# Optimization experiments

Measured on AMD Instinct MI355X. Metric: run time of the kernel, lower is better.

## Reference

```python
import jax, jax.numpy as jnp
import numpy as np

N = 100000
C = 128
H = 8
D = C // H  # head_dim = 16
E = 640000


def setup_inputs() -> dict:
    key = jax.random.key(0)
    ks = jax.random.split(key, 10)
    s = 1.0 / np.sqrt(C)
    return {
        "features": jax.random.normal(ks[0], (N, C), dtype=jnp.float32),
        "edge_index": jax.random.randint(ks[1], (2, E), 0, N, dtype=jnp.int64),
        "Wq": jax.random.uniform(ks[2], (C, C), jnp.float32, -s, s),
        "bq": jnp.zeros((C,), jnp.float32),
        "Wk": jax.random.uniform(ks[3], (C, C), jnp.float32, -s, s),
        "bk": jnp.zeros((C,), jnp.float32),
        "Wv": jax.random.uniform(ks[4], (C, C), jnp.float32, -s, s),
        "bv": jnp.zeros((C,), jnp.float32),
        "Wo": jax.random.uniform(ks[5], (C, C), jnp.float32, -s, s),
        "bo": jnp.zeros((C,), jnp.float32),
    }


def reference(features, edge_index, Wq, bq, Wk, bk, Wv, bv, Wo, bo):
    row, col = edge_index[0], edge_index[1]  # [E], [E]
    # Linear projections (torch Linear: x @ W.T + b), reshape to heads
    q = (features @ Wq.T + bq).reshape(N, H, D)
    k = (features @ Wk.T + bk).reshape(N, H, D)
    v = (features @ Wv.T + bv).reshape(N, H, D)
    # Per-edge dot-product scores [E, H]
    attn = jnp.einsum('ehd,ehd->eh', q[row], k[col]) / jnp.sqrt(jnp.float32(D))
    # Faithful to original: softmax over ALL edges (dim=0), per head
    attn = jax.nn.softmax(attn, axis=0)
    # Weighted scatter-add of source values into destination nodes
    msgs = attn[:, :, None] * v[col]  # [E, H, D]
    out = jax.ops.segment_sum(msgs, row, num_segments=N)  # [N, H, D]
    out = out.reshape(N, C)
    return out @ Wo.T + bo
```

## Files before the change

kernel.cpp:

```cpp
#include <hip/hip_runtime.h>


#define TPB 256

typedef __attribute__((ext_vector_type(8))) short short8;
typedef __attribute__((ext_vector_type(4))) short short4v;
typedef __attribute__((ext_vector_type(4))) float f32x4;

__device__ __forceinline__ short f2bf(float f) {
    unsigned u = __float_as_uint(f);
    u += 0x7fffu + ((u >> 16) & 1u);
    return (short)(u >> 16);
}
__device__ __forceinline__ float bf2f(short s) {
    return __uint_as_float(((unsigned)(unsigned short)s) << 16);
}

__global__ void wconv_kernel(const float* __restrict__ W0, const float* __restrict__ W1,
                             const float* __restrict__ W2, const float* __restrict__ W3,
                             short* __restrict__ out)
{
    int i = blockIdx.x * TPB + threadIdx.x;
    if (i >= 65536) return;
    const float* W = (i < 16384) ? W0 : (i < 32768) ? W1 : (i < 49152) ? W2 : W3;
    out[i] = f2bf(W[i & 16383]);
}

template<bool IN_BF16, bool OUT_BF16>
__device__ __forceinline__ void gemm_body(
    const void* __restrict__ Xv, int nrows,
    const short* __restrict__ Wb, const float* __restrict__ bias,
    void* __restrict__ Yv, int xblk)
{
    __shared__ short lw[16384];
    const int tid = threadIdx.x;

    short8 wreg[8];
    #pragma unroll
    for (int r = 0; r < 8; ++r) {
        int c = r * 256 + tid;
        int fragid = c >> 6, ln = c & 63;
        int n = fragid >> 2, kc = fragid & 3;
        wreg[r] = *(const short8*)&Wb[(n*16 + (ln & 15))*128 + kc*32 + (ln >> 4)*8];
    }

    const int wid = tid >> 6;
    const int lane = tid & 63;
    const int l15 = lane & 15;
    const int lh  = lane >> 4;
    const int rowbase = xblk * 128 + wid * 32;
    const int r0 = rowbase + l15, r1 = r0 + 16;
    const bool vv0 = r0 < nrows, vv1 = r1 < nrows;

    short8 xfr[4][2];
    if (IN_BF16) {
        const short* Xb = (const short*)Xv;
        #pragma unroll
        for (int kc = 0; kc < 4; ++kc) {
            xfr[kc][0] = vv0 ? *(const short8*)&Xb[(size_t)r0*128 + kc*32 + lh*8]
                             : (short8)(short)0;
            xfr[kc][1] = vv1 ? *(const short8*)&Xb[(size_t)r1*128 + kc*32 + lh*8]
                             : (short8)(short)0;
        }
    } else {
        const float* Xf = (const float*)Xv;
        const float4* P0 = (const float4*)(Xf + (size_t)r0 * 128);
        const float4* P1 = (const float4*)(Xf + (size_t)r1 * 128);
        float4 xa[4][2], xb[4][2];
        #pragma unroll
        for (int kc = 0; kc < 4; ++kc) {
            xa[kc][0] = vv0 ? P0[kc*8 + lh*2]     : make_float4(0.f,0.f,0.f,0.f);
            xb[kc][0] = vv0 ? P0[kc*8 + lh*2 + 1] : make_float4(0.f,0.f,0.f,0.f);
            xa[kc][1] = vv1 ? P1[kc*8 + lh*2]     : make_float4(0.f,0.f,0.f,0.f);
            xb[kc][1] = vv1 ? P1[kc*8 + lh*2 + 1] : make_float4(0.f,0.f,0.f,0.f);
        }
        #pragma unroll
        for (int kc = 0; kc < 4; ++kc)
            #pragma unroll
            for (int g = 0; g < 2; ++g) {
                xfr[kc][g][0] = f2bf(xa[kc][g].x);
                xfr[kc][g][1] = f2bf(xa[kc][g].y);
                xfr[kc][g][2] = f2bf(xa[kc][g].z);
                xfr[kc][g][3] = f2bf(xa[kc][g].w);
                xfr[kc][g][4] = f2bf(xb[kc][g].x);
                xfr[kc][g][5] = f2bf(xb[kc][g].y);
                xfr[kc][g][6] = f2bf(xb[kc][g].z);
                xfr[kc][g][7] = f2bf(xb[kc][g].w);
            }
    }

    #pragma unroll
    for (int r = 0; r < 8; ++r)
        *(short8*)&lw[(r * 256 + tid) * 8] = wreg[r];
    __syncthreads();

    f32x4 acc[8][2];
    #pragma unroll
    for (int n = 0; n < 8; ++n) { acc[n][0] = (f32x4)0.f; acc[n][1] = (f32x4)0.f; }

    #pragma unroll
    for (int kc = 0; kc < 4; ++kc) {
        short8 wf[8];
        #pragma unroll
        for (int n = 0; n < 8; ++n)
            wf[n] = *(const short8*)&lw[((n*4 + kc)*64 + lane) * 8];
        #pragma unroll
        for (int n = 0; n < 8; ++n) {
            acc[n][0] = __builtin_amdgcn_mfma_f32_16x16x32_bf16(wf[n], xfr[kc][0], acc[n][0], 0, 0, 0);
            acc[n][1] = __builtin_amdgcn_mfma_f32_16x16x32_bf16(wf[n], xfr[kc][1], acc[n][1], 0, 0, 0);
        }
    }

    #pragma unroll
    for (int g = 0; g < 2; ++g) {
        int row = rowbase + g*16 + l15;
        if (row >= nrows) continue;
        #pragma unroll
        for (int n = 0; n < 8; ++n) {
            float4 b4 = *(const float4*)&bias[n*16 + lh*4];
            float y0 = acc[n][g][0] + b4.x;
            float y1 = acc[n][g][1] + b4.y;
            float y2 = acc[n][g][2] + b4.z;
            float y3 = acc[n][g][3] + b4.w;
            if (OUT_BF16) {
                short4v s; s[0]=f2bf(y0); s[1]=f2bf(y1); s[2]=f2bf(y2); s[3]=f2bf(y3);
                *(short4v*)&((short*)Yv)[(size_t)row * 128 + n*16 + lh*4] = s;
            } else {
                *(float4*)&((float*)Yv)[(size_t)row * 128 + n*16 + lh*4] =
                    make_float4(y0, y1, y2, y3);
            }
        }
    }
}

__global__ __launch_bounds__(256) void gemm_out_kernel(
    const short* __restrict__ Xb, int nrows,
    const short* __restrict__ Wb, const float* __restrict__ bias,
    float* __restrict__ Y)
{
    gemm_body<true, false>(Xb, nrows, Wb, bias, Y, blockIdx.x);
}

__global__ __launch_bounds__(256) void gemm_qkv_kernel(
    const float* __restrict__ X, int nrows, int nxblk,
    const short* __restrict__ WB,
    const float* __restrict__ bq, const float* __restrict__ bk,
    const float* __restrict__ bv,
    short* __restrict__ Yb, size_t slice)
{
    int b = blockIdx.x;
    int k = b & 7, j = b >> 3;
    int jd = j / 3, w = j - 3 * jd;
    int x = k + 8 * jd;
    if (x >= nxblk) return;
    const float* bias = (w == 0) ? bq : (w == 1) ? bk : bv;
    gemm_body<false, true>(X, nrows, WB + w * 16384, bias,
                           Yb + (size_t)w * slice, x);
}

__global__ void detect_i64_kernel(const int* __restrict__ raw, int* __restrict__ flag)
{
    if (blockIdx.x == 0 && threadIdx.x == 0) {
        int odd_nonzero = 0;
        for (int i = 0; i < 128; ++i)
            if (raw[2 * i + 1] != 0) odd_nonzero = 1;
        *flag = odd_nonzero ? 0 : 1;
    }
}

__global__ void conv_hist_kernel(const void* __restrict__ raw, int E,
                                 const int* __restrict__ flag,
                                 int* __restrict__ out, int* __restrict__ deg)
{
    int i = blockIdx.x * TPB + threadIdx.x;
    if (i >= 2 * E) return;
    int v;
    if (*flag) v = (int)((const long long*)raw)[i];
    else       v = ((const int*)raw)[i];
    out[i] = v;
    if (i < E) atomicAdd(&deg[v], 1);
}

__global__ void scan1_kernel(const int* __restrict__ deg, int n,
                             int* __restrict__ rowstart, int* __restrict__ bsum)
{
    __shared__ int sm[TPB];
    int t = threadIdx.x;
    int gid = blockIdx.x * TPB + t;
    int v = (gid < n) ? deg[gid] : 0;
    sm[t] = v;
    __syncthreads();
    for (int off = 1; off < TPB; off <<= 1) {
        int x = (t >= off) ? sm[t - off] : 0;
        __syncthreads();
        sm[t] += x;
        __syncthreads();
    }
    if (gid < n) rowstart[gid] = sm[t] - v;
    if (t == TPB - 1) bsum[blockIdx.x] = sm[t];
}

__global__ void scan2_kernel(int* __restrict__ bsum, int nb)
{
    __shared__ int sm[512];
    int t = threadIdx.x;
    int v = (t < nb) ? bsum[t] : 0;
    sm[t] = v;
    __syncthreads();
    for (int off = 1; off < 512; off <<= 1) {
        int x = (t >= off) ? sm[t - off] : 0;
        __syncthreads();
        sm[t] += x;
        __syncthreads();
    }
    if (t < nb) bsum[t] = sm[t] - v;
}

__global__ void scan3_kernel(int* __restrict__ rowstart, int* __restrict__ cursor,
                             int n, int E, const int* __restrict__ bsum)
{
    int gid = blockIdx.x * TPB + threadIdx.x;
    if (gid < n) {
        int v = rowstart[gid] + bsum[blockIdx.x];
        rowstart[gid] = v;
        cursor[gid] = v;
    }
    if (gid == 0) rowstart[n] = E;
}

__global__ void fill_kernel(const int* __restrict__ ei, int E,
                            int* __restrict__ cursor, int* __restrict__ ecol)
{
    int e = blockIdx.x * TPB + threadIdx.x;
    if (e >= E) return;
    int pos = atomicAdd(&cursor[ei[e]], 1);
    ecol[pos] = ei[E + e];
}

__global__ __launch_bounds__(256) void csr_score_stats_kernel(
    const short* __restrict__ Qb, const short* __restrict__ Kb,
    const int* __restrict__ ecol, const int* __restrict__ rowstart, int N,
    float* __restrict__ S, float* __restrict__ mpart, float* __restrict__ zpart)
{
    int t = threadIdx.x;
    int idx = blockIdx.x * TPB + t;
    float m = -3.0e38f, z = 0.f;
    if (idx < N * 8) {
        int node = idx >> 3, h = idx & 7;
        const short8* q8 = (const short8*)(Qb + (size_t)node * 128 + h * 16);
        short8 q0 = q8[0], q1 = q8[1];
        int p0 = rowstart[node], p1 = rowstart[node + 1];
        if (p0 < p1) {
            const short8* kc = (const short8*)(Kb + (size_t)ecol[p0] * 128 + h * 16);
            short8 k0 = kc[0], k1 = kc[1];
            for (int p = p0; p < p1; ++p) {
                short8 k0n = k0, k1n = k1;
                if (p + 1 < p1) {
                    const short8* kn = (const short8*)(Kb + (size_t)ecol[p+1] * 128 + h * 16);
                    k0n = kn[0]; k1n = kn[1];
                }
                float dot = 0.f;
                #pragma unroll
                for (int i = 0; i < 8; ++i) {
                    dot += bf2f(q0[i]) * bf2f(k0[i]);
                    dot += bf2f(q1[i]) * bf2f(k1[i]);
                }
                float s = dot * 0.25f;
                S[(size_t)p * 8 + h] = s;
                float M = fmaxf(m, s);
                z = z * __expf(m - M) + __expf(s - M);
                m = M;
                k0 = k0n; k1 = k1n;
            }
        }
    }
    __shared__ float sm[TPB], sz[TPB];
    sm[t] = m; sz[t] = z;
    __syncthreads();
    for (int off = 128; off >= 8; off >>= 1) {
        if (t < off) {
            float m2 = sm[t + off], z2 = sz[t + off];
            float M = fmaxf(sm[t], m2);
            sz[t] = sz[t] * __expf(sm[t] - M) + z2 * __expf(m2 - M);
            sm[t] = M;
        }
        __syncthreads();
    }
    if (t < 8) {
        mpart[blockIdx.x * 8 + t] = sm[t];
        zpart[blockIdx.x * 8 + t] = sz[t];
    }
}

__global__ void stats_reduce_kernel(const float* __restrict__ mpart,
                                    const float* __restrict__ zpart,
                                    int nb, float* __restrict__ MZ)
{
    int t = threadIdx.x;
    int h = t & 7, chunk = t >> 3;
    float m = -3.0e38f, z = 0.f;
    for (int i = chunk; i < nb; i += 32) {
        float m2 = mpart[i * 8 + h], z2 = zpart[i * 8 + h];
        float M = fmaxf(m, m2);
        z = z * __expf(m - M) + z2 * __expf(m2 - M);
        m = M;
    }
    __shared__ float sm[TPB], sz[TPB];
    sm[t] = m; sz[t] = z;
    __syncthreads();
    for (int off = 128; off >= 8; off >>= 1) {
        if (t < off) {
            float m2 = sm[t + off], z2 = sz[t + off];
            float M = fmaxf(sm[t], m2);
            sz[t] = sz[t] * __expf(sm[t] - M) + z2 * __expf(m2 - M);
            sm[t] = M;
        }
        __syncthreads();
    }
    if (t < 8) { MZ[t] = sm[t]; MZ[8 + t] = sz[t]; }
}

__global__ __launch_bounds__(256) void gather_kernel(
    const float* __restrict__ S, const short* __restrict__ Vb,
    const int* __restrict__ ecol,
    const int* __restrict__ rowstart,
    const float* __restrict__ MZ, int N,
    short* __restrict__ outb)
{
    int idx = blockIdx.x * TPB + threadIdx.x;
    if (idx >= N * 8) return;
    int node = idx >> 3, h = idx & 7;
    float M = MZ[h];
    float invZ = 1.0f / MZ[8 + h];
    int p0 = rowstart[node], p1 = rowstart[node + 1];

    float a[16];
    #pragma unroll
    for (int i = 0; i < 16; ++i) a[i] = 0.f;

    if (p0 < p1) {
        const short8* vc = (const short8*)(Vb + (size_t)ecol[p0] * 128 + h * 16);
        short8 v0 = vc[0], v1 = vc[1];
        float sc = S[(size_t)p0 * 8 + h];
        for (int p = p0; p < p1; ++p) {
            short8 v0n = v0, v1n = v1;
            float sn = sc;
            if (p + 1 < p1) {
                const short8* vn = (const short8*)(Vb + (size_t)ecol[p+1] * 128 + h * 16);
                v0n = vn[0]; v1n = vn[1];
                sn = S[(size_t)(p+1) * 8 + h];
            }
            float w = __expf(sc - M) * invZ;
            #pragma unroll
            for (int i = 0; i < 8; ++i) {
                a[i]     += w * bf2f(v0[i]);
                a[8 + i] += w * bf2f(v1[i]);
            }
            v0 = v0n; v1 = v1n; sc = sn;
        }
    }
    short8 o0, o1;
    #pragma unroll
    for (int i = 0; i < 8; ++i) { o0[i] = f2bf(a[i]); o1[i] = f2bf(a[8 + i]); }
    short8* ob = (short8*)(outb + (size_t)node * 128 + h * 16);
    ob[0] = o0; ob[1] = o1;
}

extern "C" void kernel_launch(void* const* d_in, const int* in_sizes, int n_in,
                              void* d_out, int out_size, void* d_ws, size_t ws_size,
                              hipStream_t stream)
{
    const float* feat = (const float*)d_in[0];
    const void*  eraw = d_in[1];
    const float* Wq = (const float*)d_in[2];
    const float* bq = (const float*)d_in[3];
    const float* Wk = (const float*)d_in[4];
    const float* bk = (const float*)d_in[5];
    const float* Wv = (const float*)d_in[6];
    const float* bv = (const float*)d_in[7];
    const float* Wo = (const float*)d_in[8];
    const float* bo = (const float*)d_in[9];

    const int N = in_sizes[0] / 128;
    const int E = in_sizes[1] / 2;
    const size_t NC = (size_t)N * 128;
    const int EH = E * 8;
    const int gbN = (N * 8 + TPB - 1) / TPB;

    short* Qb   = (short*)d_ws;
    short* Kb   = Qb + NC;
    short* Vb   = Kb + NC;
    short* ACCb = Vb + NC;
    float* S    = (float*)(ACCb + NC);
    int*   EI   = (int*)(S + EH);
    short* WB   = (short*)(EI + 2 * E);
    float* mpart = (float*)(WB + 65536);
    float* zpart = mpart + (size_t)gbN * 8;
    float* MZ    = zpart + (size_t)gbN * 8;
    int*   flag  = (int*)(MZ + 16);
    int* deg      = flag + 16;
    int* rowstart = deg + N;
    int* cursor   = rowstart + N + 1;
    int* bsum     = cursor + N;
    int* ecol     = bsum + 512;

    const int nbS = (N + TPB - 1) / TPB;
    const int ebE = (E + TPB - 1) / TPB;

    hipMemsetAsync(deg, 0, (size_t)N * sizeof(int), stream);
    detect_i64_kernel<<<1, 64, 0, stream>>>((const int*)eraw, flag);
    conv_hist_kernel<<<(2 * E + TPB - 1) / TPB, TPB, 0, stream>>>(eraw, E, flag, EI, deg);
    scan1_kernel<<<nbS, TPB, 0, stream>>>(deg, N, rowstart, bsum);
    scan2_kernel<<<1, 512, 0, stream>>>(bsum, nbS);
    scan3_kernel<<<nbS, TPB, 0, stream>>>(rowstart, cursor, N, E, bsum);
    fill_kernel<<<ebE, TPB, 0, stream>>>(EI, E, cursor, ecol);

    wconv_kernel<<<256, TPB, 0, stream>>>(Wq, Wk, Wv, Wo, WB);
    const int gb = (N + 127) / 128;
    const int qkvgrid = 8 * 3 * ((gb + 7) / 8);
    gemm_qkv_kernel<<<qkvgrid, TPB, 0, stream>>>(feat, N, gb, WB, bq, bk, bv, Qb, NC);

    csr_score_stats_kernel<<<gbN, TPB, 0, stream>>>(Qb, Kb, ecol, rowstart, N,
                                                    S, mpart, zpart);
    stats_reduce_kernel<<<1, TPB, 0, stream>>>(mpart, zpart, gbN, MZ);

    gather_kernel<<<gbN, TPB, 0, stream>>>(S, Vb, ecol, rowstart, MZ, N, ACCb);

    gemm_out_kernel<<<gb, TPB, 0, stream>>>(ACCb, N, WB + 3 * 16384, bo, (float*)d_out);
}
```

Before: 259.3 us.

## Make projection GEMMs persistent with register prefetch of next row tile

Both the QKV and output GEMM kernels become persistent: a fixed grid (768 and 512 blocks) loads the weight tile into LDS once, then loops over row tiles with a stride. The next tile's inputs are prefetched into registers while the current tile's MFMAs run. This amortises the weight load and LDS staging over several tiles and overlaps global loads with compute, at the cost of higher register pressure and possible load imbalance across the fixed grid.

```diff
diff --git a/kernel.cpp b/kernel.cpp
--- a/kernel.cpp
+++ b/kernel.cpp
@@ -15,6 +15,12 @@
 __device__ __forceinline__ float bf2f(short s) {
     return __uint_as_float(((unsigned)(unsigned short)s) << 16);
 }
+__device__ __forceinline__ short8 cvt8(float4 a, float4 b) {
+    short8 r;
+    r[0]=f2bf(a.x); r[1]=f2bf(a.y); r[2]=f2bf(a.z); r[3]=f2bf(a.w);
+    r[4]=f2bf(b.x); r[5]=f2bf(b.y); r[6]=f2bf(b.z); r[7]=f2bf(b.w);
+    return r;
+}
 
 __global__ void wconv_kernel(const float* __restrict__ W0, const float* __restrict__ W1,
                              const float* __restrict__ W2, const float* __restrict__ W3,
@@ -27,118 +33,119 @@
 }
 
 template<bool IN_BF16, bool OUT_BF16>
-__device__ __forceinline__ void gemm_body(
-    const void* __restrict__ Xv, int nrows,
+__device__ __forceinline__ void gemm_body_pers(
+    const void* __restrict__ Xv, int nrows, int nxblk, int xstart, int xstride,
     const short* __restrict__ Wb, const float* __restrict__ bias,
-    void* __restrict__ Yv, int xblk)
+    void* __restrict__ Yv)
 {
     __shared__ short lw[16384];
     const int tid = threadIdx.x;
 
-    short8 wreg[8];
     #pragma unroll
     for (int r = 0; r < 8; ++r) {
         int c = r * 256 + tid;
         int fragid = c >> 6, ln = c & 63;
         int n = fragid >> 2, kc = fragid & 3;
-        wreg[r] = *(const short8*)&Wb[(n*16 + (ln & 15))*128 + kc*32 + (ln >> 4)*8];
-    }
+        *(short8*)&lw[c * 8] =
+            *(const short8*)&Wb[(n*16 + (ln & 15))*128 + kc*32 + (ln >> 4)*8];
+    }
+    __syncthreads();
 
     const int wid = tid >> 6;
     const int lane = tid & 63;
     const int l15 = lane & 15;
     const int lh  = lane >> 4;
-    const int rowbase = xblk * 128 + wid * 32;
-    const int r0 = rowbase + l15, r1 = r0 + 16;
-    const bool vv0 = r0 < nrows, vv1 = r1 < nrows;
-
-    short8 xfr[4][2];
-    if (IN_BF16) {
-        const short* Xb = (const short*)Xv;
+
+    float4 xa[4][2], xb[4][2];
+    short8 xr[4][2];
+
+    auto loadx = [&](int x) {
+        int rb = x * 128 + wid * 32;
+        int r0 = rb + l15, r1 = r0 + 16;
+        bool v0 = r0 < nrows, v1 = r1 < nrows;
+        if (IN_BF16) {
+            const short* Xb = (const short*)Xv;
+            #pragma unroll
+            for (int kc = 0; kc < 4; ++kc) {
+                xr[kc][0] = v0 ? *(const short8*)&Xb[(size_t)r0*128 + kc*32 + lh*8]
+                               : (short8)(short)0;
+                xr[kc][1] = v1 ? *(const short8*)&Xb[(size_t)r1*128 + kc*32 + lh*8]
+                               : (short8)(short)0;
+            }
+        } else {
+            const float* Xf = (const float*)Xv;
+            const float4* P0 = (const float4*)(Xf + (size_t)r0 * 128);
+            const float4* P1 = (const float4*)(Xf + (size_t)r1 * 128);
+            float4 z4 = make_float4(0.f, 0.f, 0.f, 0.f);
+            #pragma unroll
+            for (int kc = 0; kc < 4; ++kc) {
+                xa[kc][0] = v0 ? P0[kc*8 + lh*2]     : z4;
+                xb[kc][0] = v0 ? P0[kc*8 + lh*2 + 1] : z4;
+                xa[kc][1] = v1 ? P1[kc*8 + lh*2]     : z4;
+                xb[kc][1] = v1 ? P1[kc*8 + lh*2 + 1] : z4;
+            }
+        }
+    };
+
+    if (xstart < nxblk) loadx(xstart);
+
+    for (int x = xstart; x < nxblk; x += xstride) {
+        short8 xf[4][2];
+        if (IN_BF16) {
+            #pragma unroll
+            for (int kc = 0; kc < 4; ++kc) {
+                xf[kc][0] = xr[kc][0];
+                xf[kc][1] = xr[kc][1];
+            }
+        } else {
+            #pragma unroll
+            for (int kc = 0; kc < 4; ++kc) {
+                xf[kc][0] = cvt8(xa[kc][0], xb[kc][0]);
+                xf[kc][1] = cvt8(xa[kc][1], xb[kc][1]);
+            }
+        }
+
+        if (x + xstride < nxblk) loadx(x + xstride);
+
+        f32x4 acc[8][2];
+        #pragma unroll
+        for (int n = 0; n < 8; ++n) { acc[n][0] = (f32x4)0.f; acc[n][1] = (f32x4)0.f; }
+
         #pragma unroll
         for (int kc = 0; kc < 4; ++kc) {
-            xfr[kc][0] = vv0 ? *(const short8*)&Xb[(size_t)r0*128 + kc*32 + lh*8]
-                             : (short8)(short)0;
-            xfr[kc][1] = vv1 ? *(const short8*)&Xb[(size_t)r1*128 + kc*32 + lh*8]
-                             : (short8)(short)0;
-        }
-    } else {
-        const float* Xf = (const float*)Xv;
-        const float4* P0 = (const float4*)(Xf + (size_t)r0 * 128);
-        const float4* P1 = (const float4*)(Xf + (size_t)r1 * 128);
-        float4 xa[4][2], xb[4][2];
+            short8 wf[8];
+            #pragma unroll
+            for (int n = 0; n < 8; ++n)
+                wf[n] = *(const short8*)&lw[((n*4 + kc)*64 + lane) * 8];
+            #pragma unroll
+            for (int n = 0; n < 8; ++n) {
+                acc[n][0] = __builtin_amdgcn_mfma_f32_16x16x32_bf16(wf[n], xf[kc][0], acc[n][0], 0, 0, 0);
+                acc[n][1] = __builtin_amdgcn_mfma_f32_16x16x32_bf16(wf[n], xf[kc][1], acc[n][1], 0, 0, 0);
+            }
+        }
+
+        const int rowbase = x * 128 + wid * 32;
         #pragma unroll
-        for (int kc = 0; kc < 4; ++kc) {
-            xa[kc][0] = vv0 ? P0[kc*8 + lh*2]     : make_float4(0.f,0.f,0.f,0.f);
-            xb[kc][0] = vv0 ? P0[kc*8 + lh*2 + 1] : make_float4(0.f,0.f,0.f,0.f);
-            xa[kc][1] = vv1 ? P1[kc*8 + lh*2]     : make_float4(0.f,0.f,0.f,0.f);
-            xb[kc][1] = vv1 ? P1[kc*8 + lh*2 + 1] : make_float4(0.f,0.f,0.f,0.f);
-        }
-        #pragma unroll
-        for (int kc = 0; kc < 4; ++kc)
-            #pragma unroll
-            for (int g = 0; g < 2; ++g) {
-                xfr[kc][g][0] = f2bf(xa[kc][g].x);
-                xfr[kc][g][1] = f2bf(xa[kc][g].y);
-                xfr[kc][g][2] = f2bf(xa[kc][g].z);
-                xfr[kc][g][3] = f2bf(xa[kc][g].w);
-                xfr[kc][g][4] = f2bf(xb[kc][g].x);
-                xfr[kc][g][5] = f2bf(xb[kc][g].y);
-                xfr[kc][g][6] = f2bf(xb[kc][g].z);
-                xfr[kc][g][7] = f2bf(xb[kc][g].w);
-            }
-    }
-
-    #pragma unroll
-    for (int r = 0; r < 8; ++r)
-        *(short8*)&lw[(r * 256 + tid) * 8] = wreg[r];
-    __syncthreads();
-
-    f32x4 acc[8][2];
-    #pragma unroll
-    for (int n = 0; n < 8; ++n) { acc[n][0] = (f32x4)0.f; acc[n][1] = (f32x4)0.f; }
-
-    #pragma unroll
-    for (int kc = 0; kc < 4; ++kc) {
-        short8 wf[8];
-        #pragma unroll
-        for (int n = 0; n < 8; ++n)
-            wf[n] = *(const short8*)&lw[((n*4 + kc)*64 + lane) * 8];
-        #pragma unroll
-        for (int n = 0; n < 8; ++n) {
-            acc[n][0] = __builtin_amdgcn_mfma_f32_16x16x32_bf16(wf[n], xfr[kc][0], acc[n][0], 0, 0, 0);
-            acc[n][1] = __builtin_amdgcn_mfma_f32_16x16x32_bf16(wf[n], xfr[kc][1], acc[n][1], 0, 0, 0);
-        }
-    }
-
-    #pragma unroll
-    for (int g = 0; g < 2; ++g) {
-        int row = rowbase + g*16 + l15;
-        if (row >= nrows) continue;
-        #pragma unroll
-        for (int n = 0; n < 8; ++n) {
-            float4 b4 = *(const float4*)&bias[n*16 + lh*4];
-            float y0 = acc[n][g][0] + b4.x;
-            float y1 = acc[n][g][1] + b4.y;
-            float y2 = acc[n][g][2] + b4.z;
-            float y3 = acc[n][g][3] + b4.w;
-            if (OUT_BF16) {
-                short4v s; s[0]=f2bf(y0); s[1]=f2bf(y1); s[2]=f2bf(y2); s[3]=f2bf(y3);
-                *(short4v*)&((short*)Yv)[(size_t)row * 128 + n*16 + lh*4] = s;
-            } else {
-                *(float4*)&((float*)Yv)[(size_t)row * 128 + n*16 + lh*4] =
-                    make_float4(y0, y1, y2, y3);
-            }
-        }
-    }
-}
-
-__global__ __launch_bounds__(256) void gemm_out_kernel(
-    const short* __restrict__ Xb, int nrows,
-    const short* __restrict__ Wb, const float* __restrict__ bias,
-    float* __restrict__ Y)
-{
-    gemm_body<true, false>(Xb, nrows, Wb, bias, Y, blockIdx.x);
+        for (int g = 0; g < 2; ++g) {
+            int row = rowbase + g*16 + l15;
+            if (row >= nrows) continue;
+            #pragma unroll
+            for (int n = 0; n < 8; ++n) {
+                float4 b4 = *(const float4*)&bias[n*16 + lh*4];
+                float y0 = acc[n][g][0] + b4.x;
+                float y1 = acc[n][g][1] + b4.y;
+                float y2 = acc[n][g][2] + b4.z;
+                float y3 = acc[n][g][3] + b4.w;
+                if (OUT_BF16) {
+                    short4v s; s[0]=f2bf(y0); s[1]=f2bf(y1); s[2]=f2bf(y2); s[3]=f2bf(y3);
+                    *(short4v*)&((short*)Yv)[(size_t)row * 128 + n*16 + lh*4] = s;
+                } else {
+                    *(float4*)&((float*)Yv)[(size_t)row * 128 + n*16 + lh*4] =
+                        make_float4(y0, y1, y2, y3);
+                }
+            }
+        }
+    }
 }
 
 __global__ __launch_bounds__(256) void gemm_qkv_kernel(
@@ -149,13 +156,19 @@
     short* __restrict__ Yb, size_t slice)
 {
     int b = blockIdx.x;
-    int k = b & 7, j = b >> 3;
-    int jd = j / 3, w = j - 3 * jd;
-    int x = k + 8 * jd;
-    if (x >= nxblk) return;
+    int w = b >> 8;
+    int xstart = b & 255;
     const float* bias = (w == 0) ? bq : (w == 1) ? bk : bv;
-    gemm_body<false, true>(X, nrows, WB + w * 16384, bias,
-                           Yb + (size_t)w * slice, x);
+    gemm_body_pers<false, true>(X, nrows, nxblk, xstart, 256,
+                                WB + w * 16384, bias, Yb + (size_t)w * slice);
+}
+
+__global__ __launch_bounds__(256) void gemm_out_kernel(
+    const short* __restrict__ Xb, int nrows, int nxblk,
+    const short* __restrict__ Wb, const float* __restrict__ bias,
+    float* __restrict__ Y)
+{
+    gemm_body_pers<true, false>(Xb, nrows, nxblk, blockIdx.x, 512, Wb, bias, Y);
 }
 
 __global__ void detect_i64_kernel(const int* __restrict__ raw, int* __restrict__ flag)
@@ -417,8 +430,7 @@
 
     wconv_kernel<<<256, TPB, 0, stream>>>(Wq, Wk, Wv, Wo, WB);
     const int gb = (N + 127) / 128;
-    const int qkvgrid = 8 * 3 * ((gb + 7) / 8);
-    gemm_qkv_kernel<<<qkvgrid, TPB, 0, stream>>>(feat, N, gb, WB, bq, bk, bv, Qb, NC);
+    gemm_qkv_kernel<<<768, TPB, 0, stream>>>(feat, N, gb, WB, bq, bk, bv, Qb, NC);
 
     csr_score_stats_kernel<<<gbN, TPB, 0, stream>>>(Qb, Kb, ecol, rowstart, N,
                                                     S, mpart, zpart);
@@ -426,5 +438,5 @@
 
     gather_kernel<<<gbN, TPB, 0, stream>>>(S, Vb, ecol, rowstart, MZ, N, ACCb);
 
-    gemm_out_kernel<<<gb, TPB, 0, stream>>>(ACCb, N, WB + 3 * 16384, bo, (float*)d_out);
-}
+    gemm_out_kernel<<<512, TPB, 0, stream>>>(ACCb, N, gb, WB + 3 * 16384, bo, (float*)d_out);
+}
```

After: 284.4 us. +9.7%, slower.

## Split GEMM tiles across waves by output columns instead of rows, drop LDS

Applied to the files above, without the earlier changes.

Reworks the projection GEMMs so each block covers 32 rows and each of its four waves computes a 32-column slice, loading its weight fragments straight from global memory instead of staging all of W in shared memory behind a barrier. This removes the 32KB LDS footprint and the block-wide sync, which should raise occupancy and shorten per-block prologue. The cost is that every wave reloads the same 32 input rows (four times the X reads per block, mostly served by cache), weights are reread per block, and there are four times as many blocks.

```diff
diff --git a/kernel.cpp b/kernel.cpp
--- a/kernel.cpp
+++ b/kernel.cpp
@@ -15,6 +15,12 @@
 __device__ __forceinline__ float bf2f(short s) {
     return __uint_as_float(((unsigned)(unsigned short)s) << 16);
 }
+__device__ __forceinline__ short8 cvt8(float4 a, float4 b) {
+    short8 r;
+    r[0]=f2bf(a.x); r[1]=f2bf(a.y); r[2]=f2bf(a.z); r[3]=f2bf(a.w);
+    r[4]=f2bf(b.x); r[5]=f2bf(b.y); r[6]=f2bf(b.z); r[7]=f2bf(b.w);
+    return r;
+}
 
 __global__ void wconv_kernel(const float* __restrict__ W0, const float* __restrict__ W1,
                              const float* __restrict__ W2, const float* __restrict__ W3,
@@ -27,118 +33,90 @@
 }
 
 template<bool IN_BF16, bool OUT_BF16>
-__device__ __forceinline__ void gemm_body(
+__device__ __forceinline__ void gemm_wave_body(
     const void* __restrict__ Xv, int nrows,
     const short* __restrict__ Wb, const float* __restrict__ bias,
-    void* __restrict__ Yv, int xblk)
-{
-    __shared__ short lw[16384];
-    const int tid = threadIdx.x;
-
-    short8 wreg[8];
-    #pragma unroll
-    for (int r = 0; r < 8; ++r) {
-        int c = r * 256 + tid;
-        int fragid = c >> 6, ln = c & 63;
-        int n = fragid >> 2, kc = fragid & 3;
-        wreg[r] = *(const short8*)&Wb[(n*16 + (ln & 15))*128 + kc*32 + (ln >> 4)*8];
-    }
-
-    const int wid = tid >> 6;
+    void* __restrict__ Yv, int rtile)
+{
+    const int tid  = threadIdx.x;
+    const int wid  = tid >> 6;
     const int lane = tid & 63;
-    const int l15 = lane & 15;
-    const int lh  = lane >> 4;
-    const int rowbase = xblk * 128 + wid * 32;
+    const int l15  = lane & 15;
+    const int lh   = lane >> 4;
+    const int c0   = wid * 32;
+    const int rowbase = rtile * 32;
     const int r0 = rowbase + l15, r1 = r0 + 16;
-    const bool vv0 = r0 < nrows, vv1 = r1 < nrows;
-
-    short8 xfr[4][2];
+    const bool v0 = r0 < nrows, v1 = r1 < nrows;
+
+    short8 wf[2][4];
+    #pragma unroll
+    for (int n = 0; n < 2; ++n)
+        #pragma unroll
+        for (int kc = 0; kc < 4; ++kc)
+            wf[n][kc] = *(const short8*)&Wb[(c0 + n*16 + l15)*128 + kc*32 + lh*8];
+
+    short8 xf[2][4];
     if (IN_BF16) {
         const short* Xb = (const short*)Xv;
         #pragma unroll
         for (int kc = 0; kc < 4; ++kc) {
-            xfr[kc][0] = vv0 ? *(const short8*)&Xb[(size_t)r0*128 + kc*32 + lh*8]
-                             : (short8)(short)0;
-            xfr[kc][1] = vv1 ? *(const short8*)&Xb[(size_t)r1*128 + kc*32 + lh*8]
-                             : (short8)(short)0;
+            xf[0][kc] = v0 ? *(const short8*)&Xb[(size_t)r0*128 + kc*32 + lh*8]
+                           : (short8)(short)0;
+            xf[1][kc] = v1 ? *(const short8*)&Xb[(size_t)r1*128 + kc*32 + lh*8]
+                           : (short8)(short)0;
         }
     } else {
         const float* Xf = (const float*)Xv;
         const float4* P0 = (const float4*)(Xf + (size_t)r0 * 128);
         const float4* P1 = (const float4*)(Xf + (size_t)r1 * 128);
+        float4 z4 = make_float4(0.f, 0.f, 0.f, 0.f);
         float4 xa[4][2], xb[4][2];
         #pragma unroll
         for (int kc = 0; kc < 4; ++kc) {
-            xa[kc][0] = vv0 ? P0[kc*8 + lh*2]     : make_float4(0.f,0.f,0.f,0.f);
-            xb[kc][0] = vv0 ? P0[kc*8 + lh*2 + 1] : make_float4(0.f,0.f,0.f,0.f);
-            xa[kc][1] = vv1 ? P1[kc*8 + lh*2]     : make_float4(0.f,0.f,0.f,0.f);
-            xb[kc][1] = vv1 ? P1[kc*8 + lh*2 + 1] : make_float4(0.f,0.f,0.f,0.f);
-        }
-        #pragma unroll
-        for (int kc = 0; kc < 4; ++kc)
-            #pragma unroll
-            for (int g = 0; g < 2; ++g) {
-                xfr[kc][g][0] = f2bf(xa[kc][g].x);
-                xfr[kc][g][1] = f2bf(xa[kc][g].y);
-                xfr[kc][g][2] = f2bf(xa[kc][g].z);
-                xfr[kc][g][3] = f2bf(xa[kc][g].w);
-                xfr[kc][g][4] = f2bf(xb[kc][g].x);
-                xfr[kc][g][5] = f2bf(xb[kc][g].y);
-                xfr[kc][g][6] = f2bf(xb[kc][g].z);
-                xfr[kc][g][7] = f2bf(xb[kc][g].w);
-            }
-    }
-
-    #pragma unroll
-    for (int r = 0; r < 8; ++r)
-        *(short8*)&lw[(r * 256 + tid) * 8] = wreg[r];
-    __syncthreads();
-
-    f32x4 acc[8][2];
-    #pragma unroll
-    for (int n = 0; n < 8; ++n) { acc[n][0] = (f32x4)0.f; acc[n][1] = (f32x4)0.f; }
-
-    #pragma unroll
-    for (int kc = 0; kc < 4; ++kc) {
-        short8 wf[8];
-        #pragma unroll
-        for (int n = 0; n < 8; ++n)
-            wf[n] = *(const short8*)&lw[((n*4 + kc)*64 + lane) * 8];
-        #pragma unroll
-        for (int n = 0; n < 8; ++n) {
-            acc[n][0] = __builtin_amdgcn_mfma_f32_16x16x32_bf16(wf[n], xfr[kc][0], acc[n][0], 0, 0, 0);
-            acc[n][1] = __builtin_amdgcn_mfma_f32_16x16x32_bf16(wf[n], xfr[kc][1], acc[n][1], 0, 0, 0);
-        }
-    }
+            xa[kc][0] = v0 ? P0[kc*8 + lh*2]     : z4;
+            xb[kc][0] = v0 ? P0[kc*8 + lh*2 + 1] : z4;
+            xa[kc][1] = v1 ? P1[kc*8 + lh*2]     : z4;
+            xb[kc][1] = v1 ? P1[kc*8 + lh*2 + 1] : z4;
+        }
+        #pragma unroll
+        for (int kc = 0; kc < 4; ++kc) {
+            xf[0][kc] = cvt8(xa[kc][0], xb[kc][0]);
+            xf[1][kc] = cvt8(xa[kc][1], xb[kc][1]);
+        }
+    }
+
+    f32x4 acc[2][2];
+    #pragma unroll
+    for (int n = 0; n < 2; ++n) { acc[n][0] = (f32x4)0.f; acc[n][1] = (f32x4)0.f; }
+
+    #pragma unroll
+    for (int kc = 0; kc < 4; ++kc)
+        #pragma unroll
+        for (int n = 0; n < 2; ++n) {
+            acc[n][0] = __builtin_amdgcn_mfma_f32_16x16x32_bf16(wf[n][kc], xf[0][kc], acc[n][0], 0, 0, 0);
+            acc[n][1] = __builtin_amdgcn_mfma_f32_16x16x32_bf16(wf[n][kc], xf[1][kc], acc[n][1], 0, 0, 0);
+        }
 
     #pragma unroll
     for (int g = 0; g < 2; ++g) {
         int row = rowbase + g*16 + l15;
         if (row >= nrows) continue;
         #pragma unroll
-        for (int n = 0; n < 8; ++n) {
-            float4 b4 = *(const float4*)&bias[n*16 + lh*4];
+        for (int n = 0; n < 2; ++n) {
+            float4 b4 = *(const float4*)&bias[c0 + n*16 + lh*4];
             float y0 = acc[n][g][0] + b4.x;
             float y1 = acc[n][g][1] + b4.y;
             float y2 = acc[n][g][2] + b4.z;
             float y3 = acc[n][g][3] + b4.w;
             if (OUT_BF16) {
                 short4v s; s[0]=f2bf(y0); s[1]=f2bf(y1); s[2]=f2bf(y2); s[3]=f2bf(y3);
-                *(short4v*)&((short*)Yv)[(size_t)row * 128 + n*16 + lh*4] = s;
+                *(short4v*)&((short*)Yv)[(size_t)row * 128 + c0 + n*16 + lh*4] = s;
             } else {
-                *(float4*)&((float*)Yv)[(size_t)row * 128 + n*16 + lh*4] =
+                *(float4*)&((float*)Yv)[(size_t)row * 128 + c0 + n*16 + lh*4] =
                     make_float4(y0, y1, y2, y3);
             }
         }
     }
-}
-
-__global__ __launch_bounds__(256) void gemm_out_kernel(
-    const short* __restrict__ Xb, int nrows,
-    const short* __restrict__ Wb, const float* __restrict__ bias,
-    float* __restrict__ Y)
-{
-    gemm_body<true, false>(Xb, nrows, Wb, bias, Y, blockIdx.x);
 }
 
 __global__ __launch_bounds__(256) void gemm_qkv_kernel(
@@ -154,8 +132,16 @@
     int x = k + 8 * jd;
     if (x >= nxblk) return;
     const float* bias = (w == 0) ? bq : (w == 1) ? bk : bv;
-    gemm_body<false, true>(X, nrows, WB + w * 16384, bias,
-                           Yb + (size_t)w * slice, x);
+    gemm_wave_body<false, true>(X, nrows, WB + w * 16384, bias,
+                                Yb + (size_t)w * slice, x);
+}
+
+__global__ __launch_bounds__(256) void gemm_out_kernel(
+    const short* __restrict__ Xb, int nrows,
+    const short* __restrict__ Wb, const float* __restrict__ bias,
+    float* __restrict__ Y)
+{
+    gemm_wave_body<true, false>(Xb, nrows, Wb, bias, Y, blockIdx.x);
 }
 
 __global__ void detect_i64_kernel(const int* __restrict__ raw, int* __restrict__ flag)
@@ -416,9 +402,9 @@
     fill_kernel<<<ebE, TPB, 0, stream>>>(EI, E, cursor, ecol);
 
     wconv_kernel<<<256, TPB, 0, stream>>>(Wq, Wk, Wv, Wo, WB);
-    const int gb = (N + 127) / 128;
-    const int qkvgrid = 8 * 3 * ((gb + 7) / 8);
-    gemm_qkv_kernel<<<qkvgrid, TPB, 0, stream>>>(feat, N, gb, WB, bq, bk, bv, Qb, NC);
+    const int nxblk = (N + 31) / 32;
+    const int qkvgrid = 8 * 3 * ((nxblk + 7) / 8);
+    gemm_qkv_kernel<<<qkvgrid, TPB, 0, stream>>>(feat, N, nxblk, WB, bq, bk, bv, Qb, NC);
 
     csr_score_stats_kernel<<<gbN, TPB, 0, stream>>>(Qb, Kb, ecol, rowstart, N,
                                                     S, mpart, zpart);
@@ -426,5 +412,5 @@
 
     gather_kernel<<<gbN, TPB, 0, stream>>>(S, Vb, ecol, rowstart, MZ, N, ACCb);
 
-    gemm_out_kernel<<<gb, TPB, 0, stream>>>(ACCb, N, WB + 3 * 16384, bo, (float*)d_out);
-}
+    gemm_out_kernel<<<nxblk, TPB, 0, stream>>>(ACCb, N, WB + 3 * 16384, bo, (float*)d_out);
+}
```

After: 519.1 us. 2x slower.

## Fuse score, online softmax and value gather into one flash-style edge pass

Applied to the files above, without the earlier changes.

Merges the score/stats kernel and the gather kernel into one pass. For each node and head it keeps an online-softmax accumulation of V with a local max, and stores the unnormalized output plus that local max. A small kernel turns each local max into a per-(node, head) scale using the global max and sum, and the output GEMM applies that scale while loading its input. This removes the per-edge score buffer write and read and the second walk over the edge list and K/V gathers. In exchange the edge loop carries 16 extra accumulators with data-dependent rescaling, and the unnormalized partial sums are rounded to bf16 before scaling.

```diff
diff --git a/kernel.cpp b/kernel.cpp
--- a/kernel.cpp
+++ b/kernel.cpp
@@ -26,11 +26,10 @@
     out[i] = f2bf(W[i & 16383]);
 }
 
-template<bool IN_BF16, bool OUT_BF16>
-__device__ __forceinline__ void gemm_body(
-    const void* __restrict__ Xv, int nrows,
+__device__ __forceinline__ void gemm_body_f32in_bf16out(
+    const float* __restrict__ X, int nrows,
     const short* __restrict__ Wb, const float* __restrict__ bias,
-    void* __restrict__ Yv, int xblk)
+    short* __restrict__ Yb, int xblk)
 {
     __shared__ short lw[16384];
     const int tid = threadIdx.x;
@@ -52,42 +51,31 @@
     const int r0 = rowbase + l15, r1 = r0 + 16;
     const bool vv0 = r0 < nrows, vv1 = r1 < nrows;
 
+    const float4* P0 = (const float4*)(X + (size_t)r0 * 128);
+    const float4* P1 = (const float4*)(X + (size_t)r1 * 128);
+    float4 z4 = make_float4(0.f, 0.f, 0.f, 0.f);
+    float4 xa[4][2], xb[4][2];
+    #pragma unroll
+    for (int kc = 0; kc < 4; ++kc) {
+        xa[kc][0] = vv0 ? P0[kc*8 + lh*2]     : z4;
+        xb[kc][0] = vv0 ? P0[kc*8 + lh*2 + 1] : z4;
+        xa[kc][1] = vv1 ? P1[kc*8 + lh*2]     : z4;
+        xb[kc][1] = vv1 ? P1[kc*8 + lh*2 + 1] : z4;
+    }
     short8 xfr[4][2];
-    if (IN_BF16) {
-        const short* Xb = (const short*)Xv;
-        #pragma unroll
-        for (int kc = 0; kc < 4; ++kc) {
-            xfr[kc][0] = vv0 ? *(const short8*)&Xb[(size_t)r0*128 + kc*32 + lh*8]
-                             : (short8)(short)0;
-            xfr[kc][1] = vv1 ? *(const short8*)&Xb[(size_t)r1*128 + kc*32 + lh*8]
-                             : (short8)(short)0;
-        }
-    } else {
-        const float* Xf = (const float*)Xv;
-        const float4* P0 = (const float4*)(Xf + (size_t)r0 * 128);
-        const float4* P1 = (const float4*)(Xf + (size_t)r1 * 128);
-        float4 xa[4][2], xb[4][2];
-        #pragma unroll
-        for (int kc = 0; kc < 4; ++kc) {
-            xa[kc][0] = vv0 ? P0[kc*8 + lh*2]     : make_float4(0.f,0.f,0.f,0.f);
-            xb[kc][0] = vv0 ? P0[kc*8 + lh*2 + 1] : make_float4(0.f,0.f,0.f,0.f);
-            xa[kc][1] = vv1 ? P1[kc*8 + lh*2]     : make_float4(0.f,0.f,0.f,0.f);
-            xb[kc][1] = vv1 ? P1[kc*8 + lh*2 + 1] : make_float4(0.f,0.f,0.f,0.f);
-        }
-        #pragma unroll
-        for (int kc = 0; kc < 4; ++kc)
-            #pragma unroll
-            for (int g = 0; g < 2; ++g) {
-                xfr[kc][g][0] = f2bf(xa[kc][g].x);
-                xfr[kc][g][1] = f2bf(xa[kc][g].y);
-                xfr[kc][g][2] = f2bf(xa[kc][g].z);
-                xfr[kc][g][3] = f2bf(xa[kc][g].w);
-                xfr[kc][g][4] = f2bf(xb[kc][g].x);
-                xfr[kc][g][5] = f2bf(xb[kc][g].y);
-                xfr[kc][g][6] = f2bf(xb[kc][g].z);
-                xfr[kc][g][7] = f2bf(xb[kc][g].w);
-            }
-    }
+    #pragma unroll
+    for (int kc = 0; kc < 4; ++kc)
+        #pragma unroll
+        for (int g = 0; g < 2; ++g) {
+            xfr[kc][g][0] = f2bf(xa[kc][g].x);
+            xfr[kc][g][1] = f2bf(xa[kc][g].y);
+            xfr[kc][g][2] = f2bf(xa[kc][g].z);
+            xfr[kc][g][3] = f2bf(xa[kc][g].w);
+            xfr[kc][g][4] = f2bf(xb[kc][g].x);
+            xfr[kc][g][5] = f2bf(xb[kc][g].y);
+            xfr[kc][g][6] = f2bf(xb[kc][g].z);
+            xfr[kc][g][7] = f2bf(xb[kc][g].w);
+        }
 
     #pragma unroll
     for (int r = 0; r < 8; ++r)
@@ -118,27 +106,14 @@
         #pragma unroll
         for (int n = 0; n < 8; ++n) {
             float4 b4 = *(const float4*)&bias[n*16 + lh*4];
-            float y0 = acc[n][g][0] + b4.x;
-            float y1 = acc[n][g][1] + b4.y;
-            float y2 = acc[n][g][2] + b4.z;
-            float y3 = acc[n][g][3] + b4.w;
-            if (OUT_BF16) {
-                short4v s; s[0]=f2bf(y0); s[1]=f2bf(y1); s[2]=f2bf(y2); s[3]=f2bf(y3);
-                *(short4v*)&((short*)Yv)[(size_t)row * 128 + n*16 + lh*4] = s;
-            } else {
-                *(float4*)&((float*)Yv)[(size_t)row * 128 + n*16 + lh*4] =
-                    make_float4(y0, y1, y2, y3);
-            }
-        }
-    }
-}
-
-__global__ __launch_bounds__(256) void gemm_out_kernel(
-    const short* __restrict__ Xb, int nrows,
-    const short* __restrict__ Wb, const float* __restrict__ bias,
-    float* __restrict__ Y)
-{
-    gemm_body<true, false>(Xb, nrows, Wb, bias, Y, blockIdx.x);
+            short4v s;
+            s[0] = f2bf(acc[n][g][0] + b4.x);
+            s[1] = f2bf(acc[n][g][1] + b4.y);
+            s[2] = f2bf(acc[n][g][2] + b4.z);
+            s[3] = f2bf(acc[n][g][3] + b4.w);
+            *(short4v*)&Yb[(size_t)row * 128 + n*16 + lh*4] = s;
+        }
+    }
 }
 
 __global__ __launch_bounds__(256) void gemm_qkv_kernel(
@@ -154,8 +129,90 @@
     int x = k + 8 * jd;
     if (x >= nxblk) return;
     const float* bias = (w == 0) ? bq : (w == 1) ? bk : bv;
-    gemm_body<false, true>(X, nrows, WB + w * 16384, bias,
-                           Yb + (size_t)w * slice, x);
+    gemm_body_f32in_bf16out(X, nrows, WB + w * 16384, bias,
+                            Yb + (size_t)w * slice, x);
+}
+
+__global__ __launch_bounds__(256) void gemm_out_kernel(
+    const short* __restrict__ Xb, const float* __restrict__ sc, int nrows,
+    const short* __restrict__ Wb, const float* __restrict__ bias,
+    float* __restrict__ Y)
+{
+    __shared__ short lw[16384];
+    const int tid = threadIdx.x;
+
+    short8 wreg[8];
+    #pragma unroll
+    for (int r = 0; r < 8; ++r) {
+        int c = r * 256 + tid;
+        int fragid = c >> 6, ln = c & 63;
+        int n = fragid >> 2, kc = fragid & 3;
+        wreg[r] = *(const short8*)&Wb[(n*16 + (ln & 15))*128 + kc*32 + (ln >> 4)*8];
+    }
+
+    const int wid = tid >> 6;
+    const int lane = tid & 63;
+    const int l15 = lane & 15;
+    const int lh  = lane >> 4;
+    const int rowbase = blockIdx.x * 128 + wid * 32;
+    const int r0 = rowbase + l15, r1 = r0 + 16;
+    const bool vv0 = r0 < nrows, vv1 = r1 < nrows;
+
+    short8 xraw[4][2];
+    float  s0[4], s1[4];
+    #pragma unroll
+    for (int kc = 0; kc < 4; ++kc) {
+        xraw[kc][0] = vv0 ? *(const short8*)&Xb[(size_t)r0*128 + kc*32 + lh*8]
+                          : (short8)(short)0;
+        xraw[kc][1] = vv1 ? *(const short8*)&Xb[(size_t)r1*128 + kc*32 + lh*8]
+                          : (short8)(short)0;
+        int h = kc*2 + (lh >> 1);
+        s0[kc] = vv0 ? sc[(size_t)r0*8 + h] : 0.f;
+        s1[kc] = vv1 ? sc[(size_t)r1*8 + h] : 0.f;
+    }
+    short8 xfr[4][2];
+    #pragma unroll
+    for (int kc = 0; kc < 4; ++kc)
+        #pragma unroll
+        for (int i = 0; i < 8; ++i) {
+            xfr[kc][0][i] = f2bf(bf2f(xraw[kc][0][i]) * s0[kc]);
+            xfr[kc][1][i] = f2bf(bf2f(xraw[kc][1][i]) * s1[kc]);
+        }
+
+    #pragma unroll
+    for (int r = 0; r < 8; ++r)
+        *(short8*)&lw[(r * 256 + tid) * 8] = wreg[r];
+    __syncthreads();
+
+    f32x4 acc[8][2];
+    #pragma unroll
+    for (int n = 0; n < 8; ++n) { acc[n][0] = (f32x4)0.f; acc[n][1] = (f32x4)0.f; }
+
+    #pragma unroll
+    for (int kc = 0; kc < 4; ++kc) {
+        short8 wf[8];
+        #pragma unroll
+        for (int n = 0; n < 8; ++n)
+            wf[n] = *(const short8*)&lw[((n*4 + kc)*64 + lane) * 8];
+        #pragma unroll
+        for (int n = 0; n < 8; ++n) {
+            acc[n][0] = __builtin_amdgcn_mfma_f32_16x16x32_bf16(wf[n], xfr[kc][0], acc[n][0], 0, 0, 0);
+            acc[n][1] = __builtin_amdgcn_mfma_f32_16x16x32_bf16(wf[n], xfr[kc][1], acc[n][1], 0, 0, 0);
+        }
+    }
+
+    #pragma unroll
+    for (int g = 0; g < 2; ++g) {
+        int row = rowbase + g*16 + l15;
+        if (row >= nrows) continue;
+        #pragma unroll
+        for (int n = 0; n < 8; ++n) {
+            float4 b4 = *(const float4*)&bias[n*16 + lh*4];
+            *(float4*)&Y[(size_t)row * 128 + n*16 + lh*4] =
+                make_float4(acc[n][g][0] + b4.x, acc[n][g][1] + b4.y,
+                            acc[n][g][2] + b4.z, acc[n][g][3] + b4.w);
+        }
+    }
 }
 
 __global__ void detect_i64_kernel(const int* __restrict__ raw, int* __restrict__ flag)
@@ -237,10 +294,12 @@
     ecol[pos] = ei[E + e];
 }
 
-__global__ __launch_bounds__(256) void csr_score_stats_kernel(
+__global__ __launch_bounds__(256) void flash_edge_kernel(
     const short* __restrict__ Qb, const short* __restrict__ Kb,
+    const short* __restrict__ Vb,
     const int* __restrict__ ecol, const int* __restrict__ rowstart, int N,
-    float* __restrict__ S, float* __restrict__ mpart, float* __restrict__ zpart)
+    short* __restrict__ Ob, float* __restrict__ mloc,
+    float* __restrict__ mpart, float* __restrict__ zpart)
 {
     int t = threadIdx.x;
     int idx = blockIdx.x * TPB + t;
@@ -250,14 +309,24 @@
         const short8* q8 = (const short8*)(Qb + (size_t)node * 128 + h * 16);
         short8 q0 = q8[0], q1 = q8[1];
         int p0 = rowstart[node], p1 = rowstart[node + 1];
+
+        float o[16];
+        #pragma unroll
+        for (int i = 0; i < 16; ++i) o[i] = 0.f;
+
         if (p0 < p1) {
-            const short8* kc = (const short8*)(Kb + (size_t)ecol[p0] * 128 + h * 16);
-            short8 k0 = kc[0], k1 = kc[1];
+            int c = ecol[p0];
+            const short8* kp = (const short8*)(Kb + (size_t)c * 128 + h * 16);
+            const short8* vp = (const short8*)(Vb + (size_t)c * 128 + h * 16);
+            short8 k0 = kp[0], k1 = kp[1], v0 = vp[0], v1 = vp[1];
+
             for (int p = p0; p < p1; ++p) {
-                short8 k0n = k0, k1n = k1;
+                short8 k0n = k0, k1n = k1, v0n = v0, v1n = v1;
                 if (p + 1 < p1) {
-                    const short8* kn = (const short8*)(Kb + (size_t)ecol[p+1] * 128 + h * 16);
-                    k0n = kn[0]; k1n = kn[1];
+                    int cn = ecol[p + 1];
+                    const short8* kn = (const short8*)(Kb + (size_t)cn * 128 + h * 16);
+                    const short8* vn = (const short8*)(Vb + (size_t)cn * 128 + h * 16);
+                    k0n = kn[0]; k1n = kn[1]; v0n = vn[0]; v1n = vn[1];
                 }
                 float dot = 0.f;
                 #pragma unroll
@@ -266,14 +335,36 @@
                     dot += bf2f(q1[i]) * bf2f(k1[i]);
                 }
                 float s = dot * 0.25f;
-                S[(size_t)p * 8 + h] = s;
-                float M = fmaxf(m, s);
-                z = z * __expf(m - M) + __expf(s - M);
-                m = M;
-                k0 = k0n; k1 = k1n;
+
+                float e;
+                if (s > m) {
+                    float scl = __expf(m - s);
+                    z *= scl;
+                    #pragma unroll
+                    for (int i = 0; i < 16; ++i) o[i] *= scl;
+                    m = s;
+                    e = 1.f;
+                } else {
+                    e = __expf(s - m);
+                }
+                z += e;
+                #pragma unroll
+                for (int i = 0; i < 8; ++i) {
+                    o[i]     += e * bf2f(v0[i]);
+                    o[8 + i] += e * bf2f(v1[i]);
+                }
+                k0 = k0n; k1 = k1n; v0 = v0n; v1 = v1n;
             }
         }
-    }
+
+        short8 o0, o1;
+        #pragma unroll
+        for (int i = 0; i < 8; ++i) { o0[i] = f2bf(o[i]); o1[i] = f2bf(o[8 + i]); }
+        short8* ob = (short8*)(Ob + (size_t)node * 128 + h * 16);
+        ob[0] = o0; ob[1] = o1;
+        mloc[idx] = m;
+    }
+
     __shared__ float sm[TPB], sz[TPB];
     sm[t] = m; sz[t] = z;
     __syncthreads();
@@ -320,50 +411,14 @@
     if (t < 8) { MZ[t] = sm[t]; MZ[8 + t] = sz[t]; }
 }
 
-__global__ __launch_bounds__(256) void gather_kernel(
-    const float* __restrict__ S, const short* __restrict__ Vb,
-    const int* __restrict__ ecol,
-    const int* __restrict__ rowstart,
-    const float* __restrict__ MZ, int N,
-    short* __restrict__ outb)
+__global__ void scale_prep_kernel(const float* __restrict__ mloc,
+                                  const float* __restrict__ MZ, int total,
+                                  float* __restrict__ sc)
 {
     int idx = blockIdx.x * TPB + threadIdx.x;
-    if (idx >= N * 8) return;
-    int node = idx >> 3, h = idx & 7;
-    float M = MZ[h];
-    float invZ = 1.0f / MZ[8 + h];
-    int p0 = rowstart[node], p1 = rowstart[node + 1];
-
-    float a[16];
-    #pragma unroll
-    for (int i = 0; i < 16; ++i) a[i] = 0.f;
-
-    if (p0 < p1) {
-        const short8* vc = (const short8*)(Vb + (size_t)ecol[p0] * 128 + h * 16);
-        short8 v0 = vc[0], v1 = vc[1];
-        float sc = S[(size_t)p0 * 8 + h];
-        for (int p = p0; p < p1; ++p) {
-            short8 v0n = v0, v1n = v1;
-            float sn = sc;
-            if (p + 1 < p1) {
-                const short8* vn = (const short8*)(Vb + (size_t)ecol[p+1] * 128 + h * 16);
-                v0n = vn[0]; v1n = vn[1];
-                sn = S[(size_t)(p+1) * 8 + h];
-            }
-            float w = __expf(sc - M) * invZ;
-            #pragma unroll
-            for (int i = 0; i < 8; ++i) {
-                a[i]     += w * bf2f(v0[i]);
-                a[8 + i] += w * bf2f(v1[i]);
-            }
-            v0 = v0n; v1 = v1n; sc = sn;
-        }
-    }
-    short8 o0, o1;
-    #pragma unroll
-    for (int i = 0; i < 8; ++i) { o0[i] = f2bf(a[i]); o1[i] = f2bf(a[8 + i]); }
-    short8* ob = (short8*)(outb + (size_t)node * 128 + h * 16);
-    ob[0] = o0; ob[1] = o1;
+    if (idx >= total) return;
+    int h = idx & 7;
+    sc[idx] = __expf(mloc[idx] - MZ[h]) / MZ[8 + h];
 }
 
 extern "C" void kernel_launch(void* const* d_in, const int* in_sizes, int n_in,
@@ -384,20 +439,20 @@
     const int N = in_sizes[0] / 128;
     const int E = in_sizes[1] / 2;
     const size_t NC = (size_t)N * 128;
-    const int EH = E * 8;
     const int gbN = (N * 8 + TPB - 1) / TPB;
 
     short* Qb   = (short*)d_ws;
     short* Kb   = Qb + NC;
     short* Vb   = Kb + NC;
-    short* ACCb = Vb + NC;
-    float* S    = (float*)(ACCb + NC);
-    int*   EI   = (int*)(S + EH);
+    short* Ob   = Vb + NC;
+    int*   EI   = (int*)(Ob + NC);
     short* WB   = (short*)(EI + 2 * E);
     float* mpart = (float*)(WB + 65536);
     float* zpart = mpart + (size_t)gbN * 8;
     float* MZ    = zpart + (size_t)gbN * 8;
-    int*   flag  = (int*)(MZ + 16);
+    float* mloc  = MZ + 16;
+    float* sc    = mloc + (size_t)N * 8;
+    int*   flag  = (int*)(sc + (size_t)N * 8);
     int* deg      = flag + 16;
     int* rowstart = deg + N;
     int* cursor   = rowstart + N + 1;
@@ -420,11 +475,10 @@
     const int qkvgrid = 8 * 3 * ((gb + 7) / 8);
     gemm_qkv_kernel<<<qkvgrid, TPB, 0, stream>>>(feat, N, gb, WB, bq, bk, bv, Qb, NC);
 
-    csr_score_stats_kernel<<<gbN, TPB, 0, stream>>>(Qb, Kb, ecol, rowstart, N,
-                                                    S, mpart, zpart);
+    flash_edge_kernel<<<gbN, TPB, 0, stream>>>(Qb, Kb, Vb, ecol, rowstart, N,
+                                               Ob, mloc, mpart, zpart);
     stats_reduce_kernel<<<1, TPB, 0, stream>>>(mpart, zpart, gbN, MZ);
-
-    gather_kernel<<<gbN, TPB, 0, stream>>>(S, Vb, ecol, rowstart, MZ, N, ACCb);
-
-    gemm_out_kernel<<<gb, TPB, 0, stream>>>(ACCb, N, WB + 3 * 16384, bo, (float*)d_out);
-}
+    scale_prep_kernel<<<gbN, TPB, 0, stream>>>(mloc, MZ, N * 8, sc);
+
+    gemm_out_kernel<<<gb, TPB, 0, stream>>>(Ob, sc, N, WB + 3 * 16384, bo, (float*)d_out);
+}
```

Result: slower. 299.3 us (+15.4%).
